# Kernel tuning notes

Hardware: AMD Instinct MI355X
Metric: run time of the kernel (lower is better)

The kernel has to match this reference:

```python
import jax, jax.numpy as jnp
import numpy as np

DIM = 1024
N_EXPERTS = 8
TOP_K = 2
B, S = 2, 1024


def setup_inputs() -> dict:
    key = jax.random.key(0)
    ks = jax.random.split(key, 4)
    scale = 0.02
    return {
        "u_t": jax.random.normal(ks[0], (B, S, DIM), dtype=jnp.float32),
        "centroids": jax.random.normal(ks[1], (N_EXPERTS, DIM), dtype=jnp.float32),
        "score_biases": jnp.zeros((N_EXPERTS,), dtype=jnp.float32),
        "W1": jax.random.normal(ks[2], (N_EXPERTS, DIM, 4 * DIM), dtype=jnp.float32) * scale,
        "b1": jnp.zeros((N_EXPERTS, 4 * DIM), dtype=jnp.float32),
        "W2": jax.random.normal(ks[3], (N_EXPERTS, 4 * DIM, DIM), dtype=jnp.float32) * scale,
        "b2": jnp.zeros((N_EXPERTS, DIM), dtype=jnp.float32),
    }


def reference(u_t, centroids, score_biases, W1, b1, W2, b2):
    Bs, Ss, dim = u_t.shape
    T = Bs * Ss
    N = centroids.shape[0]
    K = TOP_K

    u_flat = u_t.reshape(T, dim)
    scores = u_flat @ centroids.T + score_biases          # [T, N]
    gate = jax.nn.softmax(scores, axis=-1)                # [T, N]
    topk_vals, topk_idx = jax.lax.top_k(gate, K)          # [T, K]

    flat_idx = topk_idx.reshape(-1)                       # [T*K]

    # load-violation stats (no grad path; pure counts)
    perfect_load = K * T / N
    f_i = jnp.zeros((N,), dtype=jnp.float32).at[flat_idx].add(1.0)
    maxvio = (jnp.max(f_i) - perfect_load) / perfect_load

    # Grouped MLP expressed as dense per-expert compute over all tokens,
    # then combined with a sparse [T, N] gate matrix (same math as masked dispatch).
    h = jax.nn.relu(jnp.einsum("td,ndh->nth", u_flat, W1) + b1[:, None, :])  # [N, T, 4*dim]
    expert_outs = jnp.einsum("nth,nhd->ntd", h, W2) + b2[:, None, :]          # [N, T, dim]

    rows = jnp.repeat(jnp.arange(T), K)
    combine_w = jnp.zeros((T, N), dtype=topk_vals.dtype).at[rows, flat_idx].add(topk_vals.reshape(-1))
    out = jnp.einsum("tn,ntd->td", combine_w, expert_outs).reshape(Bs, Ss, dim)
    return (out, maxvio)
```

## Files before the change

kernel.cpp:

```cpp
#include <hip/hip_runtime.h>
#include <hip/hip_bf16.h>

#define T_TOK 2048
#define DIMS  1024
#define HID   4096
#define NE    8
#define BM 128
#define BN 128
#define BK 64

typedef __bf16 bf16x8 __attribute__((ext_vector_type(8)));
typedef float  f32x4  __attribute__((ext_vector_type(4)));

__device__ __forceinline__ unsigned short f2bf(float f) {
  unsigned u = __float_as_uint(f);
  u += 0x7FFFu + ((u >> 16) & 1u);
  return (unsigned short)(u >> 16);
}
__device__ __forceinline__ float bf2f(unsigned short s) {
  return __uint_as_float(((unsigned)s) << 16);
}

__device__ __forceinline__ void g2l16(const void* g, void* l) {
  __builtin_amdgcn_global_load_lds((const __attribute__((address_space(1))) void*)g,
                                   (__attribute__((address_space(3))) void*)l,
                                   16, 0, 0);
}

__device__ __forceinline__ void transcode_tile(const float* __restrict__ src,
    unsigned short* __restrict__ dst, int src_ld, int dst_ld, int r0, int c0,
    unsigned short* lds, int tid) {
  int rbase = tid >> 5;
  int c4l = (tid & 31) * 4;
#pragma unroll 4
  for (int it = 0; it < 16; it++) {
    int r = rbase + it * 8;
    float4 v = *(const float4*)(src + (size_t)(r0 + r) * src_ld + c0 + c4l);
    unsigned short b[4];
    b[0] = f2bf(v.x); b[1] = f2bf(v.y); b[2] = f2bf(v.z); b[3] = f2bf(v.w);
#pragma unroll
    for (int j = 0; j < 4; j++) {
      int c = c4l + j;
      int chunk = it ^ ((c >> 2) & 15);
      lds[c * 128 + chunk * 8 + rbase] = b[j];
    }
  }
  __syncthreads();
  int ck = tid & 15;
  int cb = tid >> 4;
#pragma unroll 4
  for (int it = 0; it < 8; it++) {
    int c = cb + it * 16;
    int chunk = ck ^ ((c >> 2) & 15);
    uint4 v = *(const uint4*)(&lds[c * 128 + chunk * 8]);
    *(uint4*)(dst + (size_t)(c0 + c) * dst_ld + r0 + ck * 8) = v;
  }
}

__global__ __launch_bounds__(256) void k_route(const float* __restrict__ u,
    const float* __restrict__ cent, const float* __restrict__ sbias,
    int* __restrict__ topk_idx, float* __restrict__ topk_val,
    unsigned short* __restrict__ ub,
    const float* __restrict__ W1, unsigned short* __restrict__ w1t) {
  __shared__ __align__(16) unsigned short tlds[128 * 128];
  if (blockIdx.x >= 512) {
    int rank = (int)blockIdx.x - 512;
    int te = rank >> 8, tt = rank & 255;
    int r0 = (tt & 7) * 128, c0 = (tt >> 3) * 128;
    transcode_tile(W1 + (size_t)te * DIMS * HID, w1t + (size_t)te * HID * DIMS,
                   HID, DIMS, r0, c0, tlds, threadIdx.x);
    return;
  }
  int wave = threadIdx.x >> 6;
  int lane = threadIdx.x & 63;
  int t = blockIdx.x * 4 + wave;
  const float* ur = u + (size_t)t * DIMS;
  float p[NE];
#pragma unroll
  for (int n = 0; n < NE; n++) p[n] = 0.f;
#pragma unroll
  for (int ch = 0; ch < 4; ch++) {
    int d = ch * 256 + lane * 4;
    float4 uv = *(const float4*)(ur + d);
    ushort4 o4;
    o4.x = f2bf(uv.x); o4.y = f2bf(uv.y); o4.z = f2bf(uv.z); o4.w = f2bf(uv.w);
    *(ushort4*)(ub + (size_t)t * DIMS + d) = o4;
#pragma unroll
    for (int n = 0; n < NE; n++) {
      float4 cv = *(const float4*)(cent + n * DIMS + d);
      p[n] += uv.x * cv.x + uv.y * cv.y + uv.z * cv.z + uv.w * cv.w;
    }
  }
#pragma unroll
  for (int n = 0; n < NE; n++) {
#pragma unroll
    for (int o = 32; o > 0; o >>= 1) p[n] += __shfl_xor(p[n], o);
  }
  if (lane == 0) {
    float g[NE];
    float m = -1e30f;
#pragma unroll
    for (int n = 0; n < NE; n++) { g[n] = p[n] + sbias[n]; m = fmaxf(m, g[n]); }
    float sum = 0.f;
#pragma unroll
    for (int n = 0; n < NE; n++) { g[n] = expf(g[n] - m); sum += g[n]; }
    float inv = 1.f / sum;
#pragma unroll
    for (int n = 0; n < NE; n++) g[n] *= inv;
    int i0 = 0;
#pragma unroll
    for (int n = 1; n < NE; n++) if (g[n] > g[i0]) i0 = n;
    int i1 = (i0 == 0) ? 1 : 0;
#pragma unroll
    for (int n = 0; n < NE; n++) if (n != i0 && g[n] > g[i1]) i1 = n;
    topk_idx[2 * t] = i0;     topk_idx[2 * t + 1] = i1;
    topk_val[2 * t] = g[i0];  topk_val[2 * t + 1] = g[i1];
  }
}

__global__ __launch_bounds__(256) void k_finalize(const int* __restrict__ topk_idx,
    int* __restrict__ cnt, int* __restrict__ offs, float* __restrict__ maxvio,
    int* __restrict__ rowtok, int* __restrict__ pairpos) {
  __shared__ int lc[NE], lcur[NE];
  int tid = threadIdx.x;
  if (tid < NE) lc[tid] = 0;
  __syncthreads();
#pragma unroll
  for (int i = 0; i < 16; i++) {
    int e = topk_idx[tid * 16 + i];
    atomicAdd(&lc[e], 1);
  }
  __syncthreads();
  if (tid == 0) {
    int o = 0, mx = 0;
#pragma unroll
    for (int n = 0; n < NE; n++) {
      int c = lc[n];
      cnt[n] = c; offs[n] = o; lcur[n] = o;
      o += c; mx = max(mx, c);
    }
    maxvio[0] = ((float)mx - 512.f) / 512.f;
  }
  __syncthreads();
#pragma unroll
  for (int i = 0; i < 8; i++) {
    int t = tid + i * 256;
#pragma unroll
    for (int k = 0; k < 2; k++) {
      int e = topk_idx[2 * t + k];
      int pos = atomicAdd(&lcur[e], 1);
      rowtok[pos] = t;
      pairpos[2 * t + k] = pos;
    }
  }
}

__global__ __launch_bounds__(256) void k_gemm1n(const unsigned short* __restrict__ ub,
    const unsigned short* __restrict__ w1t, const float* __restrict__ b1,
    const int* __restrict__ rowtok, const int* __restrict__ cnts, const int* __restrict__ offs,
    unsigned short* __restrict__ h,
    const float* __restrict__ W2, unsigned short* __restrict__ w2t) {
  __shared__ __align__(16) unsigned char smem[65536];
  int tid = threadIdx.x;
  int e = blockIdx.z;
  int cnt = cnts[e];
  int m0 = blockIdx.y * BM;

  if (m0 >= cnt) {
    int live[NE];
#pragma unroll
    for (int z = 0; z < NE; z++) live[z] = min(16, (cnts[z] + BM - 1) >> 7);
    int rank = 0;
    for (int z = 0; z < e; z++) rank += (16 - live[z]) * 32;
    rank += ((int)blockIdx.y - live[e]) * 32 + (int)blockIdx.x;
    if (rank >= 2048) return;
    int te = rank >> 8, tt = rank & 255;
    transcode_tile(W2 + (size_t)te * HID * DIMS, w2t + (size_t)te * HID * DIMS,
                   DIMS, HID, (tt & 31) * 128, (tt >> 5) * 128,
                   (unsigned short*)smem, tid);
    return;
  }

  int off = offs[e];
  int n0 = blockIdx.x * BN;
  int lane = tid & 63;
  int wm = (tid >> 7) & 1;
  int wn = (tid >> 6) & 1;
  int srow = tid >> 3;
  int cp = tid & 7;
  const unsigned short* gA[4];
  const unsigned short* gB[4];
#pragma unroll
  for (int a = 0; a < 4; a++) {
    int r = a * 32 + srow;
    int c = cp ^ (r & 7);
    int pr = min(off + m0 + r, off + cnt - 1);
    int tok = rowtok[pr];
    gA[a] = ub + (size_t)tok * DIMS + c * 8;
    gB[a] = w1t + ((size_t)e * HID + (n0 + r)) * DIMS + c * 8;
  }
  unsigned wboff = (unsigned)__builtin_amdgcn_readfirstlane((tid >> 6) << 10);
  f32x4 acc[4][4];
  f32x4 zz = {0.f, 0.f, 0.f, 0.f};
#pragma unroll
  for (int i = 0; i < 4; i++)
#pragma unroll
    for (int j = 0; j < 4; j++) acc[i][j] = zz;

  int lane15 = lane & 15, quad = lane >> 4, l7 = lane & 7;
  unsigned aOff = (unsigned)((wm * 64 + lane15) * 128);
  unsigned bOff = (unsigned)(16384 + (wn * 64 + lane15) * 128);

#pragma unroll
  for (int a = 0; a < 4; a++) g2l16(gA[a], smem + a * 4096 + wboff);
#pragma unroll
  for (int a = 0; a < 4; a++) g2l16(gB[a], smem + 16384 + a * 4096 + wboff);

#pragma unroll 1
  for (int it = 0; it < DIMS / BK; it++) {
    unsigned base = (unsigned)((it & 1) << 15);
    unsigned nb = base ^ 32768u;
    if (it + 1 < DIMS / BK) {
      int k1 = (it + 1) * BK;
#pragma unroll
      for (int a = 0; a < 4; a++) g2l16(gA[a] + k1, smem + nb + a * 4096 + wboff);
#pragma unroll
      for (int a = 0; a < 4; a++) g2l16(gB[a] + k1, smem + nb + 16384 + a * 4096 + wboff);
      asm volatile("s_waitcnt vmcnt(8)" ::: "memory");
    } else {
      asm volatile("s_waitcnt vmcnt(0)" ::: "memory");
    }
    __builtin_amdgcn_s_barrier();
    __builtin_amdgcn_sched_barrier(0);
#pragma unroll
    for (int s = 0; s < 2; s++) {
      unsigned cpf = (unsigned)(((s * 4 + quad) ^ l7) * 16);
      bf16x8 af[4], bfr[4];
#pragma unroll
      for (int i = 0; i < 4; i++) af[i] = *(const bf16x8*)(smem + base + aOff + i * 2048 + cpf);
#pragma unroll
      for (int j = 0; j < 4; j++) bfr[j] = *(const bf16x8*)(smem + base + bOff + j * 2048 + cpf);
#pragma unroll
      for (int i = 0; i < 4; i++)
#pragma unroll
        for (int j = 0; j < 4; j++)
          acc[i][j] = __builtin_amdgcn_mfma_f32_16x16x32_bf16(af[i], bfr[j], acc[i][j], 0, 0, 0);
    }
    __builtin_amdgcn_sched_barrier(0);
    asm volatile("s_waitcnt lgkmcnt(0)" ::: "memory");
    __builtin_amdgcn_s_barrier();
  }
  float b1v[4];
#pragma unroll
  for (int j = 0; j < 4; j++) b1v[j] = b1[e * HID + n0 + wn * 64 + j * 16 + lane15];
#pragma unroll
  for (int i = 0; i < 4; i++) {
#pragma unroll
    for (int r = 0; r < 4; r++) {
      int mrow = m0 + wm * 64 + i * 16 + quad * 4 + r;
      if (mrow < cnt) {
        size_t hrow = (size_t)(off + mrow) * HID;
#pragma unroll
        for (int j = 0; j < 4; j++) {
          int col = n0 + wn * 64 + j * 16 + lane15;
          float v = fmaxf(acc[i][j][r] + b1v[j], 0.f);
          h[hrow + col] = f2bf(v);
        }
      }
    }
  }
}

__global__ __launch_bounds__(256) void k_gemm1o(const unsigned short* __restrict__ ub,
    const float* __restrict__ W1, const float* __restrict__ b1,
    const int* __restrict__ rowtok, const int* __restrict__ cnts, const int* __restrict__ offs,
    unsigned short* __restrict__ h,
    const float* __restrict__ W2, unsigned short* __restrict__ w2t) {
  __shared__ __align__(16) unsigned char smem[32768];
  int tid = threadIdx.x;
  int e = blockIdx.z;
  int cnt = cnts[e];
  int m0 = blockIdx.y * BM;

  if (m0 >= cnt) {
    int live[NE];
#pragma unroll
    for (int z = 0; z < NE; z++) live[z] = min(16, (cnts[z] + BM - 1) >> 7);
    int rank = 0;
    for (int z = 0; z < e; z++) rank += (16 - live[z]) * 32;
    rank += ((int)blockIdx.y - live[e]) * 32 + (int)blockIdx.x;
    if (rank >= 2048) return;
    int te = rank >> 8, tt = rank & 255;
    transcode_tile(W2 + (size_t)te * HID * DIMS, w2t + (size_t)te * HID * DIMS,
                   DIMS, HID, (tt & 31) * 128, (tt >> 5) * 128,
                   (unsigned short*)smem, tid);
    return;
  }

  int off = offs[e];
  int n0 = blockIdx.x * BN;
  int lane = tid & 63;
  int wv = tid >> 6;
  int wm = (tid >> 7) & 1;
  int wn = (tid >> 6) & 1;
  int srow = tid >> 3;
  int cp = tid & 7;
  const float* w1e = W1 + (size_t)e * DIMS * HID;
  const unsigned short* gAp[4];
#pragma unroll
  for (int a = 0; a < 4; a++) {
    int r = a * 32 + srow;
    int c = cp ^ (r & 7);
    int pr = min(off + m0 + r, off + cnt - 1);
    int tok = rowtok[pr];
    gAp[a] = ub + (size_t)tok * DIMS + c * 8;
  }
  int wboff = __builtin_amdgcn_readfirstlane(wv << 10);
  f32x4 acc[4][4];
  f32x4 zz = {0.f, 0.f, 0.f, 0.f};
#pragma unroll
  for (int i = 0; i < 4; i++)
#pragma unroll
    for (int j = 0; j < 4; j++) acc[i][j] = zz;

  int lane15 = lane & 15, quad = lane >> 4, l7 = lane & 7;
  unsigned aRowOff = (unsigned)((wm * 64 + lane15) * 128);
  unsigned bRowOff = (unsigned)(16384 + (wn * 64 + lane15) * 128);

#pragma unroll 1
  for (int k0 = 0; k0 < DIMS; k0 += BK) {
#pragma unroll
    for (int a = 0; a < 4; a++) g2l16(gAp[a] + k0, smem + a * 4096 + wboff);
#pragma unroll
    for (int jj = 0; jj < 4; jj++) {
      int j = wv * 4 + jj;
      int kc = j & 7, nh = j >> 3;
      int nloc = nh * 64 + lane;
      const float* src = w1e + (size_t)(k0 + kc * 8) * HID + n0 + nloc;
      float t0, t1, t2, t3, t4, t5, t6, t7;
      t0 = src[0];            t1 = src[(size_t)HID];
      t2 = src[(size_t)2 * HID]; t3 = src[(size_t)3 * HID];
      t4 = src[(size_t)4 * HID]; t5 = src[(size_t)5 * HID];
      t6 = src[(size_t)6 * HID]; t7 = src[(size_t)7 * HID];
      bf16x8 pk;
      pk[0] = (__bf16)t0; pk[1] = (__bf16)t1; pk[2] = (__bf16)t2; pk[3] = (__bf16)t3;
      pk[4] = (__bf16)t4; pk[5] = (__bf16)t5; pk[6] = (__bf16)t6; pk[7] = (__bf16)t7;
      int cs = kc ^ (lane & 7);
      *(bf16x8*)(smem + 16384 + nloc * 128 + cs * 16) = pk;
    }
    __syncthreads();
#pragma unroll
    for (int s = 0; s < 2; s++) {
      unsigned cpf = (unsigned)(((s * 4 + quad) ^ l7) * 16);
      bf16x8 af[4], bfr[4];
#pragma unroll
      for (int i = 0; i < 4; i++) af[i] = *(const bf16x8*)(smem + aRowOff + i * 2048 + cpf);
#pragma unroll
      for (int j = 0; j < 4; j++) bfr[j] = *(const bf16x8*)(smem + bRowOff + j * 2048 + cpf);
#pragma unroll
      for (int i = 0; i < 4; i++)
#pragma unroll
        for (int j = 0; j < 4; j++)
          acc[i][j] = __builtin_amdgcn_mfma_f32_16x16x32_bf16(af[i], bfr[j], acc[i][j], 0, 0, 0);
    }
    __syncthreads();
  }
  float b1v[4];
#pragma unroll
  for (int j = 0; j < 4; j++) b1v[j] = b1[e * HID + n0 + wn * 64 + j * 16 + lane15];
#pragma unroll
  for (int i = 0; i < 4; i++) {
#pragma unroll
    for (int r = 0; r < 4; r++) {
      int mrow = m0 + wm * 64 + i * 16 + quad * 4 + r;
      if (mrow < cnt) {
        size_t hrow = (size_t)(off + mrow) * HID;
#pragma unroll
        for (int j = 0; j < 4; j++) {
          int col = n0 + wn * 64 + j * 16 + lane15;
          float v = fmaxf(acc[i][j][r] + b1v[j], 0.f);
          h[hrow + col] = f2bf(v);
        }
      }
    }
  }
}

__global__ __launch_bounds__(256) void k_gemm2(const unsigned short* __restrict__ hbuf,
    const unsigned short* __restrict__ w2t, const float* __restrict__ b2,
    const int* __restrict__ cnts, const int* __restrict__ offs,
    unsigned short* __restrict__ pout, int KC) {
  int z = blockIdx.z;
  int e = z & 7;
  int sp = z >> 3;
  int cnt = cnts[e];
  int m0 = blockIdx.y * BM;
  if (m0 >= cnt) return;
  int off = offs[e];
  int n0 = blockIdx.x * BN;
  __shared__ __align__(16) unsigned char smem[65536];

  int tid = threadIdx.x;
  int lane = tid & 63;
  int wm = (tid >> 7) & 1;
  int wn = (tid >> 6) & 1;
  int srow = tid >> 3;
  int cp = tid & 7;
  const unsigned short* gA[4];
  const unsigned short* gB[4];
#pragma unroll
  for (int a = 0; a < 4; a++) {
    int r = a * 32 + srow;
    int c = cp ^ (r & 7);
    int pr = min(off + m0 + r, off + cnt - 1);
    gA[a] = hbuf + (size_t)pr * HID + c * 8;
    gB[a] = w2t + ((size_t)e * DIMS + (n0 + r)) * HID + c * 8;
  }
  unsigned wboff = (unsigned)__builtin_amdgcn_readfirstlane((tid >> 6) << 10);
  f32x4 acc[4][4];
  f32x4 zz = {0.f, 0.f, 0.f, 0.f};
#pragma unroll
  for (int i = 0; i < 4; i++)
#pragma unroll
    for (int j = 0; j < 4; j++) acc[i][j] = zz;

  int lane15 = lane & 15, quad = lane >> 4, l7 = lane & 7;
  unsigned aOff = (unsigned)((wm * 64 + lane15) * 128);
  unsigned bOff = (unsigned)(16384 + (wn * 64 + lane15) * 128);

  int kbeg = sp * KC;
  int NIT = KC / BK;
#pragma unroll
  for (int a = 0; a < 4; a++) g2l16(gA[a] + kbeg, smem + a * 4096 + wboff);
#pragma unroll
  for (int a = 0; a < 4; a++) g2l16(gB[a] + kbeg, smem + 16384 + a * 4096 + wboff);

#pragma unroll 1
  for (int it = 0; it < NIT; it++) {
    unsigned base = (unsigned)((it & 1) << 15);
    unsigned nb = base ^ 32768u;
    if (it + 1 < NIT) {
      int k1 = kbeg + (it + 1) * BK;
#pragma unroll
      for (int a = 0; a < 4; a++) g2l16(gA[a] + k1, smem + nb + a * 4096 + wboff);
#pragma unroll
      for (int a = 0; a < 4; a++) g2l16(gB[a] + k1, smem + nb + 16384 + a * 4096 + wboff);
      asm volatile("s_waitcnt vmcnt(8)" ::: "memory");
    } else {
      asm volatile("s_waitcnt vmcnt(0)" ::: "memory");
    }
    __builtin_amdgcn_s_barrier();
    __builtin_amdgcn_sched_barrier(0);
#pragma unroll
    for (int s = 0; s < 2; s++) {
      unsigned cpf = (unsigned)(((s * 4 + quad) ^ l7) * 16);
      bf16x8 af[4], bfr[4];
#pragma unroll
      for (int i = 0; i < 4; i++) af[i] = *(const bf16x8*)(smem + base + aOff + i * 2048 + cpf);
#pragma unroll
      for (int j = 0; j < 4; j++) bfr[j] = *(const bf16x8*)(smem + base + bOff + j * 2048 + cpf);
#pragma unroll
      for (int i = 0; i < 4; i++)
#pragma unroll
        for (int j = 0; j < 4; j++)
          acc[i][j] = __builtin_amdgcn_mfma_f32_16x16x32_bf16(af[i], bfr[j], acc[i][j], 0, 0, 0);
    }
    __builtin_amdgcn_sched_barrier(0);
    asm volatile("s_waitcnt lgkmcnt(0)" ::: "memory");
    __builtin_amdgcn_s_barrier();
  }
  float b2v[4];
#pragma unroll
  for (int j = 0; j < 4; j++)
    b2v[j] = (sp == 0) ? b2[e * DIMS + n0 + wn * 64 + j * 16 + lane15] : 0.f;
  unsigned short* pme = pout + (size_t)sp * T_TOK * 2 * DIMS;
#pragma unroll
  for (int i = 0; i < 4; i++) {
#pragma unroll
    for (int r = 0; r < 4; r++) {
      int mrow = m0 + wm * 64 + i * 16 + quad * 4 + r;
      if (mrow < cnt) {
        size_t prow = (size_t)(off + mrow) * DIMS;
#pragma unroll
        for (int j = 0; j < 4; j++) {
          int col = n0 + wn * 64 + j * 16 + lane15;
          pme[prow + col] = f2bf(acc[i][j][r] + b2v[j]);
        }
      }
    }
  }
}

__global__ __launch_bounds__(256) void k_combine(const unsigned short* __restrict__ pout,
    const int* __restrict__ pairpos, const float* __restrict__ tkv,
    float* __restrict__ out, int nsplit) {
  int t = blockIdx.x;
  int d = threadIdx.x * 4;
  int p0 = pairpos[2 * t], p1 = pairpos[2 * t + 1];
  float w0 = tkv[2 * t], w1 = tkv[2 * t + 1];
  float a0 = 0.f, a1 = 0.f, a2 = 0.f, a3 = 0.f;
  float c0 = 0.f, c1 = 0.f, c2 = 0.f, c3 = 0.f;
  const size_t SS = (size_t)T_TOK * 2 * DIMS;
  for (int s = 0; s < nsplit; s++) {
    ushort4 av = *(const ushort4*)(pout + s * SS + (size_t)p0 * DIMS + d);
    ushort4 bv = *(const ushort4*)(pout + s * SS + (size_t)p1 * DIMS + d);
    a0 += bf2f(av.x); a1 += bf2f(av.y); a2 += bf2f(av.z); a3 += bf2f(av.w);
    c0 += bf2f(bv.x); c1 += bf2f(bv.y); c2 += bf2f(bv.z); c3 += bf2f(bv.w);
  }
  float4 o;
  o.x = w0 * a0 + w1 * c0;
  o.y = w0 * a1 + w1 * c1;
  o.z = w0 * a2 + w1 * c2;
  o.w = w0 * a3 + w1 * c3;
  *(float4*)(out + (size_t)t * DIMS + d) = o;
}

extern "C" void kernel_launch(void* const* d_in, const int* in_sizes, int n_in,
                              void* d_out, int out_size, void* d_ws, size_t ws_size,
                              hipStream_t stream) {
  const float* u     = (const float*)d_in[0];
  const float* cent  = (const float*)d_in[1];
  const float* sbias = (const float*)d_in[2];
  const float* W1    = (const float*)d_in[3];
  const float* b1    = (const float*)d_in[4];
  const float* W2    = (const float*)d_in[5];
  const float* b2    = (const float*)d_in[6];
  float* out = (float*)d_out;

  char* ws = (char*)d_ws;
  unsigned short* ubuf = (unsigned short*)(ws);
  unsigned short* hbuf = (unsigned short*)(ws + 4194304);
  unsigned short* w2t  = (unsigned short*)(ws + 37748736);
  const size_t REG4 = 104857600ull;
  const size_t PSZ = (size_t)T_TOK * 2 * DIMS * 2;
  const size_t NEED_NEW = REG4 + 67108864ull + 1048576ull;

  if (ws_size >= NEED_NEW) {
    unsigned short* w1t   = (unsigned short*)(ws + REG4);
    unsigned short* poutb = (unsigned short*)(ws + REG4);
    const int nsplit = 2;
    char* r = ws + REG4 + 67108864ull;
    int*   cnt      = (int*)(r);
    int*   offs     = (int*)(r + 64);
    int*   topk_idx = (int*)(r + 256);
    float* topk_val = (float*)(r + 256 + 16384);
    int*   rowtok   = (int*)(r + 256 + 32768);
    int*   pairpos  = (int*)(r + 256 + 49152);

    k_route<<<2560, 256, 0, stream>>>(u, cent, sbias, topk_idx, topk_val, ubuf, W1, w1t);
    k_finalize<<<1, 256, 0, stream>>>(topk_idx, cnt, offs, out + 2097152, rowtok, pairpos);
    k_gemm1n<<<dim3(32, 16, 8), 256, 0, stream>>>(ubuf, w1t, b1, rowtok, cnt, offs, hbuf,
                                                  W2, w2t);
    k_gemm2<<<dim3(8, 16, 8 * nsplit), 256, 0, stream>>>(hbuf, w2t, b2, cnt, offs,
                                                         poutb, HID / nsplit);
    k_combine<<<2048, 256, 0, stream>>>(poutb, pairpos, topk_val, out, nsplit);
  } else {
    int nsplit = (ws_size >= REG4 + 4 * PSZ + (1u << 20)) ? 4 : 1;
    unsigned short* poutb = (unsigned short*)(ws + REG4);
    char* r = ws + REG4 + (size_t)nsplit * PSZ;
    int*   cnt      = (int*)(r);
    int*   offs     = (int*)(r + 64);
    int*   topk_idx = (int*)(r + 256);
    float* topk_val = (float*)(r + 256 + 16384);
    int*   rowtok   = (int*)(r + 256 + 32768);
    int*   pairpos  = (int*)(r + 256 + 49152);

    k_route<<<512, 256, 0, stream>>>(u, cent, sbias, topk_idx, topk_val, ubuf, W1, ubuf);
    k_finalize<<<1, 256, 0, stream>>>(topk_idx, cnt, offs, out + 2097152, rowtok, pairpos);
    k_gemm1o<<<dim3(32, 16, 8), 256, 0, stream>>>(ubuf, W1, b1, rowtok, cnt, offs, hbuf,
                                                  W2, w2t);
    k_gemm2<<<dim3(8, 16, 8 * nsplit), 256, 0, stream>>>(hbuf, w2t, b2, cnt, offs,
                                                         poutb, HID / nsplit);
    k_combine<<<2048, 256, 0, stream>>>(poutb, pairpos, topk_val, out, nsplit);
  }
}
```

Before: 430.2 us.

## Enlarge expert GEMM tiles to 256x256 with 512 threads and scan-based finalize

Both expert GEMMs move from 128x128 tiles with 4 waves to 256x256 tiles with 8 waves, each wave now holding an 8x4 MFMA accumulator block, and use 128KB of LDS with double buffering. Idle gemm1 blocks now loop to transcode several W2 tiles each, covering the smaller grid. The split-K factor for gemm2 rises to 4 to keep enough blocks. k_finalize replaces shared-memory atomics with a prefix scan, giving a deterministic token ordering. The larger tiles raise operand reuse and arithmetic intensity but cut occupancy, increase register pressure, and waste more work on partially filled expert tiles.

After: 503.5 us. 17.0% more time.

```diff
diff --git a/kernel.cpp b/kernel.cpp
--- a/kernel.cpp
+++ b/kernel.cpp
@@ -5,9 +5,6 @@
 #define DIMS  1024
 #define HID   4096
 #define NE    8
-#define BM 128
-#define BN 128
-#define BK 64
 
 typedef __bf16 bf16x8 __attribute__((ext_vector_type(8)));
 typedef float  f32x4  __attribute__((ext_vector_type(4)));
@@ -121,55 +118,194 @@
 __global__ __launch_bounds__(256) void k_finalize(const int* __restrict__ topk_idx,
     int* __restrict__ cnt, int* __restrict__ offs, float* __restrict__ maxvio,
     int* __restrict__ rowtok, int* __restrict__ pairpos) {
-  __shared__ int lc[NE], lcur[NE];
+  __shared__ int sc[256][NE];
+  __shared__ int sof[NE];
   int tid = threadIdx.x;
-  if (tid < NE) lc[tid] = 0;
+  int el[16];
+  int c[NE];
+#pragma unroll
+  for (int n = 0; n < NE; n++) c[n] = 0;
+#pragma unroll
+  for (int i = 0; i < 16; i++) {
+    el[i] = topk_idx[tid * 16 + i];
+#pragma unroll
+    for (int n = 0; n < NE; n++) c[n] += (el[i] == n) ? 1 : 0;
+  }
+#pragma unroll
+  for (int n = 0; n < NE; n++) sc[tid][n] = c[n];
   __syncthreads();
-#pragma unroll
-  for (int i = 0; i < 16; i++) {
-    int e = topk_idx[tid * 16 + i];
-    atomicAdd(&lc[e], 1);
-  }
-  __syncthreads();
+  for (int st = 1; st < 256; st <<= 1) {
+    int v[NE];
+#pragma unroll
+    for (int n = 0; n < NE; n++) v[n] = (tid >= st) ? sc[tid - st][n] : 0;
+    __syncthreads();
+#pragma unroll
+    for (int n = 0; n < NE; n++) sc[tid][n] += v[n];
+    __syncthreads();
+  }
   if (tid == 0) {
     int o = 0, mx = 0;
 #pragma unroll
     for (int n = 0; n < NE; n++) {
-      int c = lc[n];
-      cnt[n] = c; offs[n] = o; lcur[n] = o;
-      o += c; mx = max(mx, c);
+      int t = sc[255][n];
+      cnt[n] = t; offs[n] = o; sof[n] = o;
+      o += t; mx = max(mx, t);
     }
     maxvio[0] = ((float)mx - 512.f) / 512.f;
   }
   __syncthreads();
-#pragma unroll
-  for (int i = 0; i < 8; i++) {
-    int t = tid + i * 256;
-#pragma unroll
-    for (int k = 0; k < 2; k++) {
-      int e = topk_idx[2 * t + k];
-      int pos = atomicAdd(&lcur[e], 1);
-      rowtok[pos] = t;
-      pairpos[2 * t + k] = pos;
-    }
-  }
-}
-
-__global__ __launch_bounds__(256) void k_gemm1n(const unsigned short* __restrict__ ub,
+  int base[NE];
+#pragma unroll
+  for (int n = 0; n < NE; n++) base[n] = sof[n] + sc[tid][n] - c[n];
+#pragma unroll
+  for (int i = 0; i < 16; i++) {
+    int eN = el[i];
+    int pos = 0;
+#pragma unroll
+    for (int n = 0; n < NE; n++) if (eN == n) { pos = base[n]; base[n] = pos + 1; }
+    rowtok[pos] = (tid * 16 + i) >> 1;
+    pairpos[tid * 16 + i] = pos;
+  }
+}
+
+__global__ __launch_bounds__(512) void k_gemm1n(const unsigned short* __restrict__ ub,
     const unsigned short* __restrict__ w1t, const float* __restrict__ b1,
     const int* __restrict__ rowtok, const int* __restrict__ cnts, const int* __restrict__ offs,
     unsigned short* __restrict__ h,
     const float* __restrict__ W2, unsigned short* __restrict__ w2t) {
-  __shared__ __align__(16) unsigned char smem[65536];
+  __shared__ __align__(16) unsigned char smem[131072];
   int tid = threadIdx.x;
   int e = blockIdx.z;
   int cnt = cnts[e];
-  int m0 = blockIdx.y * BM;
+  int m0 = blockIdx.y * 256;
 
   if (m0 >= cnt) {
     int live[NE];
-#pragma unroll
-    for (int z = 0; z < NE; z++) live[z] = min(16, (cnts[z] + BM - 1) >> 7);
+    int nlive = 0;
+#pragma unroll
+    for (int z = 0; z < NE; z++) { live[z] = min(8, (cnts[z] + 255) >> 8); nlive += live[z]; }
+    int rank = 0;
+    for (int z = 0; z < e; z++) rank += (8 - live[z]) * 16;
+    rank += ((int)blockIdx.y - live[e]) * 16 + (int)blockIdx.x;
+    int nidle = (64 - nlive) * 16;
+    if (nidle < 1) nidle = 1;
+    int hh = tid >> 8;
+    unsigned short* lds = (unsigned short*)smem + hh * 16384;
+    for (int tt = rank * 2 + hh; tt < 2048; tt += nidle * 2) {
+      int te = tt >> 8, t2 = tt & 255;
+      transcode_tile(W2 + (size_t)te * HID * DIMS, w2t + (size_t)te * HID * DIMS,
+                     DIMS, HID, (t2 & 31) * 128, (t2 >> 5) * 128, lds, tid & 255);
+      __syncthreads();
+    }
+    return;
+  }
+
+  int off = offs[e];
+  int n0 = blockIdx.x * 256;
+  int lane = tid & 63;
+  int wv = tid >> 6;
+  int wm = wv >> 2;
+  int wn = wv & 3;
+  int srow = tid >> 3;
+  int cp = tid & 7;
+  const unsigned short* gA[4];
+  const unsigned short* gB[4];
+#pragma unroll
+  for (int a = 0; a < 4; a++) {
+    int r = a * 64 + srow;
+    int c = cp ^ (r & 7);
+    int pr = min(off + m0 + r, off + cnt - 1);
+    int tok = rowtok[pr];
+    gA[a] = ub + (size_t)tok * DIMS + c * 8;
+    gB[a] = w1t + ((size_t)e * HID + (n0 + r)) * DIMS + c * 8;
+  }
+  unsigned wboff = (unsigned)__builtin_amdgcn_readfirstlane(wv << 10);
+  f32x4 acc[8][4];
+  f32x4 zz = {0.f, 0.f, 0.f, 0.f};
+#pragma unroll
+  for (int i = 0; i < 8; i++)
+#pragma unroll
+    for (int j = 0; j < 4; j++) acc[i][j] = zz;
+
+  int lane15 = lane & 15, quad = lane >> 4, l7 = lane & 7;
+  unsigned aOff = (unsigned)((wm * 128 + lane15) * 128);
+  unsigned bOff = (unsigned)(32768 + (wn * 64 + lane15) * 128);
+
+#pragma unroll
+  for (int a = 0; a < 4; a++) g2l16(gA[a], smem + a * 8192 + wboff);
+#pragma unroll
+  for (int a = 0; a < 4; a++) g2l16(gB[a], smem + 32768 + a * 8192 + wboff);
+
+#pragma unroll 1
+  for (int it = 0; it < 16; it++) {
+    unsigned base = (unsigned)((it & 1) << 16);
+    unsigned nb = base ^ 65536u;
+    if (it + 1 < 16) {
+      int k1 = (it + 1) * 64;
+#pragma unroll
+      for (int a = 0; a < 4; a++) g2l16(gA[a] + k1, smem + nb + a * 8192 + wboff);
+#pragma unroll
+      for (int a = 0; a < 4; a++) g2l16(gB[a] + k1, smem + nb + 32768 + a * 8192 + wboff);
+      asm volatile("s_waitcnt vmcnt(8)" ::: "memory");
+    } else {
+      asm volatile("s_waitcnt vmcnt(0)" ::: "memory");
+    }
+    __builtin_amdgcn_s_barrier();
+    __builtin_amdgcn_sched_barrier(0);
+#pragma unroll
+    for (int s = 0; s < 2; s++) {
+      unsigned cpf = (unsigned)(((s * 4 + quad) ^ l7) * 16);
+      bf16x8 af[8], bfr[4];
+#pragma unroll
+      for (int i = 0; i < 8; i++) af[i] = *(const bf16x8*)(smem + base + aOff + i * 2048 + cpf);
+#pragma unroll
+      for (int j = 0; j < 4; j++) bfr[j] = *(const bf16x8*)(smem + base + bOff + j * 2048 + cpf);
+#pragma unroll
+      for (int i = 0; i < 8; i++)
+#pragma unroll
+        for (int j = 0; j < 4; j++)
+          acc[i][j] = __builtin_amdgcn_mfma_f32_16x16x32_bf16(af[i], bfr[j], acc[i][j], 0, 0, 0);
+    }
+    __builtin_amdgcn_sched_barrier(0);
+    asm volatile("s_waitcnt lgkmcnt(0)" ::: "memory");
+    __builtin_amdgcn_s_barrier();
+  }
+  float b1v[4];
+#pragma unroll
+  for (int j = 0; j < 4; j++) b1v[j] = b1[e * HID + n0 + wn * 64 + j * 16 + lane15];
+#pragma unroll
+  for (int i = 0; i < 8; i++) {
+#pragma unroll
+    for (int r = 0; r < 4; r++) {
+      int mrow = m0 + wm * 128 + i * 16 + quad * 4 + r;
+      if (mrow < cnt) {
+        size_t hrow = (size_t)(off + mrow) * HID;
+#pragma unroll
+        for (int j = 0; j < 4; j++) {
+          int col = n0 + wn * 64 + j * 16 + lane15;
+          float v = fmaxf(acc[i][j][r] + b1v[j], 0.f);
+          h[hrow + col] = f2bf(v);
+        }
+      }
+    }
+  }
+}
+
+__global__ __launch_bounds__(256) void k_gemm1o(const unsigned short* __restrict__ ub,
+    const float* __restrict__ W1, const float* __restrict__ b1,
+    const int* __restrict__ rowtok, const int* __restrict__ cnts, const int* __restrict__ offs,
+    unsigned short* __restrict__ h,
+    const float* __restrict__ W2, unsigned short* __restrict__ w2t) {
+  __shared__ __align__(16) unsigned char smem[32768];
+  int tid = threadIdx.x;
+  int e = blockIdx.z;
+  int cnt = cnts[e];
+  int m0 = blockIdx.y * 128;
+
+  if (m0 >= cnt) {
+    int live[NE];
+#pragma unroll
+    for (int z = 0; z < NE; z++) live[z] = min(16, (cnts[z] + 127) >> 7);
     int rank = 0;
     for (int z = 0; z < e; z++) rank += (16 - live[z]) * 32;
     rank += ((int)blockIdx.y - live[e]) * 32 + (int)blockIdx.x;
@@ -182,123 +318,7 @@
   }
 
   int off = offs[e];
-  int n0 = blockIdx.x * BN;
-  int lane = tid & 63;
-  int wm = (tid >> 7) & 1;
-  int wn = (tid >> 6) & 1;
-  int srow = tid >> 3;
-  int cp = tid & 7;
-  const unsigned short* gA[4];
-  const unsigned short* gB[4];
-#pragma unroll
-  for (int a = 0; a < 4; a++) {
-    int r = a * 32 + srow;
-    int c = cp ^ (r & 7);
-    int pr = min(off + m0 + r, off + cnt - 1);
-    int tok = rowtok[pr];
-    gA[a] = ub + (size_t)tok * DIMS + c * 8;
-    gB[a] = w1t + ((size_t)e * HID + (n0 + r)) * DIMS + c * 8;
-  }
-  unsigned wboff = (unsigned)__builtin_amdgcn_readfirstlane((tid >> 6) << 10);
-  f32x4 acc[4][4];
-  f32x4 zz = {0.f, 0.f, 0.f, 0.f};
-#pragma unroll
-  for (int i = 0; i < 4; i++)
-#pragma unroll
-    for (int j = 0; j < 4; j++) acc[i][j] = zz;
-
-  int lane15 = lane & 15, quad = lane >> 4, l7 = lane & 7;
-  unsigned aOff = (unsigned)((wm * 64 + lane15) * 128);
-  unsigned bOff = (unsigned)(16384 + (wn * 64 + lane15) * 128);
-
-#pragma unroll
-  for (int a = 0; a < 4; a++) g2l16(gA[a], smem + a * 4096 + wboff);
-#pragma unroll
-  for (int a = 0; a < 4; a++) g2l16(gB[a], smem + 16384 + a * 4096 + wboff);
-
-#pragma unroll 1
-  for (int it = 0; it < DIMS / BK; it++) {
-    unsigned base = (unsigned)((it & 1) << 15);
-    unsigned nb = base ^ 32768u;
-    if (it + 1 < DIMS / BK) {
-      int k1 = (it + 1) * BK;
-#pragma unroll
-      for (int a = 0; a < 4; a++) g2l16(gA[a] + k1, smem + nb + a * 4096 + wboff);
-#pragma unroll
-      for (int a = 0; a < 4; a++) g2l16(gB[a] + k1, smem + nb + 16384 + a * 4096 + wboff);
-      asm volatile("s_waitcnt vmcnt(8)" ::: "memory");
-    } else {
-      asm volatile("s_waitcnt vmcnt(0)" ::: "memory");
-    }
-    __builtin_amdgcn_s_barrier();
-    __builtin_amdgcn_sched_barrier(0);
-#pragma unroll
-    for (int s = 0; s < 2; s++) {
-      unsigned cpf = (unsigned)(((s * 4 + quad) ^ l7) * 16);
-      bf16x8 af[4], bfr[4];
-#pragma unroll
-      for (int i = 0; i < 4; i++) af[i] = *(const bf16x8*)(smem + base + aOff + i * 2048 + cpf);
-#pragma unroll
-      for (int j = 0; j < 4; j++) bfr[j] = *(const bf16x8*)(smem + base + bOff + j * 2048 + cpf);
-#pragma unroll
-      for (int i = 0; i < 4; i++)
-#pragma unroll
-        for (int j = 0; j < 4; j++)
-          acc[i][j] = __builtin_amdgcn_mfma_f32_16x16x32_bf16(af[i], bfr[j], acc[i][j], 0, 0, 0);
-    }
-    __builtin_amdgcn_sched_barrier(0);
-    asm volatile("s_waitcnt lgkmcnt(0)" ::: "memory");
-    __builtin_amdgcn_s_barrier();
-  }
-  float b1v[4];
-#pragma unroll
-  for (int j = 0; j < 4; j++) b1v[j] = b1[e * HID + n0 + wn * 64 + j * 16 + lane15];
-#pragma unroll
-  for (int i = 0; i < 4; i++) {
-#pragma unroll
-    for (int r = 0; r < 4; r++) {
-      int mrow = m0 + wm * 64 + i * 16 + quad * 4 + r;
-      if (mrow < cnt) {
-        size_t hrow = (size_t)(off + mrow) * HID;
-#pragma unroll
-        for (int j = 0; j < 4; j++) {
-          int col = n0 + wn * 64 + j * 16 + lane15;
-          float v = fmaxf(acc[i][j][r] + b1v[j], 0.f);
-          h[hrow + col] = f2bf(v);
-        }
-      }
-    }
-  }
-}
-
-__global__ __launch_bounds__(256) void k_gemm1o(const unsigned short* __restrict__ ub,
-    const float* __restrict__ W1, const float* __restrict__ b1,
-    const int* __restrict__ rowtok, const int* __restrict__ cnts, const int* __restrict__ offs,
-    unsigned short* __restrict__ h,
-    const float* __restrict__ W2, unsigned short* __restrict__ w2t) {
-  __shared__ __align__(16) unsigned char smem[32768];
-  int tid = threadIdx.x;
-  int e = blockIdx.z;
-  int cnt = cnts[e];
-  int m0 = blockIdx.y * BM;
-
-  if (m0 >= cnt) {
-    int live[NE];
-#pragma unroll
-    for (int z = 0; z < NE; z++) live[z] = min(16, (cnts[z] + BM - 1) >> 7);
-    int rank = 0;
-    for (int z = 0; z < e; z++) rank += (16 - live[z]) * 32;
-    rank += ((int)blockIdx.y - live[e]) * 32 + (int)blockIdx.x;
-    if (rank >= 2048) return;
-    int te = rank >> 8, tt = rank & 255;
-    transcode_tile(W2 + (size_t)te * HID * DIMS, w2t + (size_t)te * HID * DIMS,
-                   DIMS, HID, (tt & 31) * 128, (tt >> 5) * 128,
-                   (unsigned short*)smem, tid);
-    return;
-  }
-
-  int off = offs[e];
-  int n0 = blockIdx.x * BN;
+  int n0 = blockIdx.x * 128;
   int lane = tid & 63;
   int wv = tid >> 6;
   int wm = (tid >> 7) & 1;
@@ -328,7 +348,7 @@
   unsigned bRowOff = (unsigned)(16384 + (wn * 64 + lane15) * 128);
 
 #pragma unroll 1
-  for (int k0 = 0; k0 < DIMS; k0 += BK) {
+  for (int k0 = 0; k0 < DIMS; k0 += 64) {
 #pragma unroll
     for (int a = 0; a < 4; a++) g2l16(gAp[a] + k0, smem + a * 4096 + wboff);
 #pragma unroll
@@ -386,7 +406,7 @@
   }
 }
 
-__global__ __launch_bounds__(256) void k_gemm2(const unsigned short* __restrict__ hbuf,
+__global__ __launch_bounds__(512) void k_gemm2(const unsigned short* __restrict__ hbuf,
     const unsigned short* __restrict__ w2t, const float* __restrict__ b2,
     const int* __restrict__ cnts, const int* __restrict__ offs,
     unsigned short* __restrict__ pout, int KC) {
@@ -394,57 +414,58 @@
   int e = z & 7;
   int sp = z >> 3;
   int cnt = cnts[e];
-  int m0 = blockIdx.y * BM;
+  int m0 = blockIdx.y * 256;
   if (m0 >= cnt) return;
   int off = offs[e];
-  int n0 = blockIdx.x * BN;
-  __shared__ __align__(16) unsigned char smem[65536];
+  int n0 = blockIdx.x * 256;
+  __shared__ __align__(16) unsigned char smem[131072];
 
   int tid = threadIdx.x;
   int lane = tid & 63;
-  int wm = (tid >> 7) & 1;
-  int wn = (tid >> 6) & 1;
+  int wv = tid >> 6;
+  int wm = wv >> 2;
+  int wn = wv & 3;
   int srow = tid >> 3;
   int cp = tid & 7;
   const unsigned short* gA[4];
   const unsigned short* gB[4];
 #pragma unroll
   for (int a = 0; a < 4; a++) {
-    int r = a * 32 + srow;
+    int r = a * 64 + srow;
     int c = cp ^ (r & 7);
     int pr = min(off + m0 + r, off + cnt - 1);
     gA[a] = hbuf + (size_t)pr * HID + c * 8;
     gB[a] = w2t + ((size_t)e * DIMS + (n0 + r)) * HID + c * 8;
   }
-  unsigned wboff = (unsigned)__builtin_amdgcn_readfirstlane((tid >> 6) << 10);
-  f32x4 acc[4][4];
+  unsigned wboff = (unsigned)__builtin_amdgcn_readfirstlane(wv << 10);
+  f32x4 acc[8][4];
   f32x4 zz = {0.f, 0.f, 0.f, 0.f};
 #pragma unroll
-  for (int i = 0; i < 4; i++)
+  for (int i = 0; i < 8; i++)
 #pragma unroll
     for (int j = 0; j < 4; j++) acc[i][j] = zz;
 
   int lane15 = lane & 15, quad = lane >> 4, l7 = lane & 7;
-  unsigned aOff = (unsigned)((wm * 64 + lane15) * 128);
-  unsigned bOff = (unsigned)(16384 + (wn * 64 + lane15) * 128);
+  unsigned aOff = (unsigned)((wm * 128 + lane15) * 128);
+  unsigned bOff = (unsigned)(32768 + (wn * 64 + lane15) * 128);
 
   int kbeg = sp * KC;
-  int NIT = KC / BK;
-#pragma unroll
-  for (int a = 0; a < 4; a++) g2l16(gA[a] + kbeg, smem + a * 4096 + wboff);
-#pragma unroll
-  for (int a = 0; a < 4; a++) g2l16(gB[a] + kbeg, smem + 16384 + a * 4096 + wboff);
+  int NIT = KC / 64;
+#pragma unroll
+  for (int a = 0; a < 4; a++) g2l16(gA[a] + kbeg, smem + a * 8192 + wboff);
+#pragma unroll
+  for (int a = 0; a < 4; a++) g2l16(gB[a] + kbeg, smem + 32768 + a * 8192 + wboff);
 
 #pragma unroll 1
   for (int it = 0; it < NIT; it++) {
-    unsigned base = (unsigned)((it & 1) << 15);
-    unsigned nb = base ^ 32768u;
+    unsigned base = (unsigned)((it & 1) << 16);
+    unsigned nb = base ^ 65536u;
     if (it + 1 < NIT) {
-      int k1 = kbeg + (it + 1) * BK;
-#pragma unroll
-      for (int a = 0; a < 4; a++) g2l16(gA[a] + k1, smem + nb + a * 4096 + wboff);
-#pragma unroll
-      for (int a = 0; a < 4; a++) g2l16(gB[a] + k1, smem + nb + 16384 + a * 4096 + wboff);
+      int k1 = kbeg + (it + 1) * 64;
+#pragma unroll
+      for (int a = 0; a < 4; a++) g2l16(gA[a] + k1, smem + nb + a * 8192 + wboff);
+#pragma unroll
+      for (int a = 0; a < 4; a++) g2l16(gB[a] + k1, smem + nb + 32768 + a * 8192 + wboff);
       asm volatile("s_waitcnt vmcnt(8)" ::: "memory");
     } else {
       asm volatile("s_waitcnt vmcnt(0)" ::: "memory");
@@ -454,13 +475,13 @@
 #pragma unroll
     for (int s = 0; s < 2; s++) {
       unsigned cpf = (unsigned)(((s * 4 + quad) ^ l7) * 16);
-      bf16x8 af[4], bfr[4];
-#pragma unroll
-      for (int i = 0; i < 4; i++) af[i] = *(const bf16x8*)(smem + base + aOff + i * 2048 + cpf);
+      bf16x8 af[8], bfr[4];
+#pragma unroll
+      for (int i = 0; i < 8; i++) af[i] = *(const bf16x8*)(smem + base + aOff + i * 2048 + cpf);
 #pragma unroll
       for (int j = 0; j < 4; j++) bfr[j] = *(const bf16x8*)(smem + base + bOff + j * 2048 + cpf);
 #pragma unroll
-      for (int i = 0; i < 4; i++)
+      for (int i = 0; i < 8; i++)
 #pragma unroll
         for (int j = 0; j < 4; j++)
           acc[i][j] = __builtin_amdgcn_mfma_f32_16x16x32_bf16(af[i], bfr[j], acc[i][j], 0, 0, 0);
@@ -475,10 +496,10 @@
     b2v[j] = (sp == 0) ? b2[e * DIMS + n0 + wn * 64 + j * 16 + lane15] : 0.f;
   unsigned short* pme = pout + (size_t)sp * T_TOK * 2 * DIMS;
 #pragma unroll
-  for (int i = 0; i < 4; i++) {
+  for (int i = 0; i < 8; i++) {
 #pragma unroll
     for (int r = 0; r < 4; r++) {
-      int mrow = m0 + wm * 64 + i * 16 + quad * 4 + r;
+      int mrow = m0 + wm * 128 + i * 16 + quad * 4 + r;
       if (mrow < cnt) {
         size_t prow = (size_t)(off + mrow) * DIMS;
 #pragma unroll
@@ -538,7 +559,7 @@
   if (ws_size >= NEED_NEW) {
     unsigned short* w1t   = (unsigned short*)(ws + REG4);
     unsigned short* poutb = (unsigned short*)(ws + REG4);
-    const int nsplit = 2;
+    const int nsplit = 4;
     char* r = ws + REG4 + 67108864ull;
     int*   cnt      = (int*)(r);
     int*   offs     = (int*)(r + 64);
@@ -549,10 +570,10 @@
 
     k_route<<<2560, 256, 0, stream>>>(u, cent, sbias, topk_idx, topk_val, ubuf, W1, w1t);
     k_finalize<<<1, 256, 0, stream>>>(topk_idx, cnt, offs, out + 2097152, rowtok, pairpos);
-    k_gemm1n<<<dim3(32, 16, 8), 256, 0, stream>>>(ubuf, w1t, b1, rowtok, cnt, offs, hbuf,
-                                                  W2, w2t);
-    k_gemm2<<<dim3(8, 16, 8 * nsplit), 256, 0, stream>>>(hbuf, w2t, b2, cnt, offs,
-                                                         poutb, HID / nsplit);
+    k_gemm1n<<<dim3(16, 8, 8), 512, 0, stream>>>(ubuf, w1t, b1, rowtok, cnt, offs, hbuf,
+                                                 W2, w2t);
+    k_gemm2<<<dim3(4, 8, 8 * nsplit), 512, 0, stream>>>(hbuf, w2t, b2, cnt, offs,
+                                                        poutb, HID / nsplit);
     k_combine<<<2048, 256, 0, stream>>>(poutb, pairpos, topk_val, out, nsplit);
   } else {
     int nsplit = (ws_size >= REG4 + 4 * PSZ + (1u << 20)) ? 4 : 1;
@@ -569,8 +590,8 @@
     k_finalize<<<1, 256, 0, stream>>>(topk_idx, cnt, offs, out + 2097152, rowtok, pairpos);
     k_gemm1o<<<dim3(32, 16, 8), 256, 0, stream>>>(ubuf, W1, b1, rowtok, cnt, offs, hbuf,
                                                   W2, w2t);
-    k_gemm2<<<dim3(8, 16, 8 * nsplit), 256, 0, stream>>>(hbuf, w2t, b2, cnt, offs,
-                                                         poutb, HID / nsplit);
+    k_gemm2<<<dim3(4, 8, 8 * nsplit), 512, 0, stream>>>(hbuf, w2t, b2, cnt, offs,
+                                                        poutb, HID / nsplit);
     k_combine<<<2048, 256, 0, stream>>>(poutb, pairpos, topk_val, out, nsplit);
   }
 }
```
